# Performance work log

Measured on AMD Instinct MI355X. Metric: run time of the kernel, lower is better.

## Reference

```python
import jax, jax.numpy as jnp
import numpy as np
import math

B, T, D, H = 4, 2048, 1024, 16
DH = D // H

def setup_inputs() -> dict:
    key = jax.random.key(0)
    ks = jax.random.split(key, 12)
    s = 1.0 / math.sqrt(D)
    inp = {
        'q': jax.random.normal(ks[0], (B, T, D), jnp.float32),
        'k': jax.random.normal(ks[1], (B, T, D), jnp.float32),
        'v': jax.random.normal(ks[2], (B, T, D), jnp.float32),
        # causal attn_mask [B, Tq, Tk]; all-keep padding mask [B,1,1,Tk]
        'attn_mask': jnp.broadcast_to(jnp.tril(jnp.ones((T, T), jnp.bool_)), (B, T, T)),
        'key_keep_mask': jnp.ones((B, 1, 1, T), jnp.bool_),
        'wq_w': jax.random.normal(ks[3], (D, D), jnp.float32) * s,
        'wq_b': jnp.zeros((D,), jnp.float32),
        'wk_w': jax.random.normal(ks[4], (D, D), jnp.float32) * s,
        'wk_b': jnp.zeros((D,), jnp.float32),
        'wv_w': jax.random.normal(ks[5], (D, D), jnp.float32) * s,
        'wv_b': jnp.zeros((D,), jnp.float32),
        'wo_w': jax.random.normal(ks[6], (D, D), jnp.float32) * s,
        'wo_b': jnp.zeros((D,), jnp.float32),
    }
    return inp

def reference(q, k, v, attn_mask, key_keep_mask, wq_w, wq_b, wk_w, wk_b, wv_w, wv_b, wo_w, wo_b):
    # projections (torch Linear: x @ W^T + b)
    Q = (q @ wq_w.T + wq_b).reshape(B, -1, H, DH).transpose(0, 2, 1, 3)  # [B,H,Tq,DH]
    K = (k @ wk_w.T + wk_b).reshape(B, -1, H, DH).transpose(0, 2, 1, 3)
    V = (v @ wv_w.T + wv_b).reshape(B, -1, H, DH).transpose(0, 2, 1, 3)
    scores = jnp.einsum('bhqd,bhkd->bhqk', Q, K) / math.sqrt(DH)
    neg_inf = jnp.array(-jnp.inf, scores.dtype)
    scores = jnp.where(attn_mask[:, None, :, :], scores, neg_inf)
    scores = jnp.where(key_keep_mask, scores, neg_inf)
    attn = jax.nn.softmax(scores, axis=-1)  # dropout p=0 -> identity
    out = jnp.einsum('bhqk,bhkd->bhqd', attn, V)
    out = out.transpose(0, 2, 1, 3).reshape(B, -1, D)
    return out @ wo_w.T + wo_b
```

## Files before the change

### kernel.cpp

```cpp
#include <hip/hip_runtime.h>
#include <cstdint>
#include <cstddef>


typedef float f32x4 __attribute__((ext_vector_type(4)));
typedef short bf16x8 __attribute__((ext_vector_type(8)));
typedef float fltx4 __attribute__((ext_vector_type(4)));
typedef unsigned short u16x4 __attribute__((ext_vector_type(4)));

#define GLOBAL_AS __attribute__((address_space(1)))
#define LDS_AS __attribute__((address_space(3)))

__device__ __forceinline__ unsigned short f2bf(float f) {
    union { float f; unsigned int u; } x;
    x.f = f;
    unsigned int u = x.u;
    unsigned int r = (u + 0x7FFFu + ((u >> 16) & 1u)) >> 16;
    return (unsigned short)r;
}

__device__ __forceinline__ unsigned int pack_trunc(float a, float b) {
    union { float f; unsigned int u; } x, y;
    x.f = a; y.f = b;
    return (x.u >> 16) | (y.u & 0xFFFF0000u);
}

__global__ __launch_bounds__(256) void cast_all_kernel(
    const float* __restrict__ q, const float* __restrict__ k, const float* __restrict__ v,
    const float* __restrict__ wq, const float* __restrict__ wk,
    const float* __restrict__ wv, const float* __restrict__ wo,
    unsigned short* __restrict__ dst)
{
    const size_t SEG = 8388608;
    const size_t WSEG = 1048576;
    size_t i = ((size_t)blockIdx.x * 256 + threadIdx.x) * 4;
    const float* src;
    size_t off;
    if (i < SEG)               { src = q;  off = i; }
    else if (i < 2 * SEG)      { src = k;  off = i - SEG; }
    else if (i < 3 * SEG)      { src = v;  off = i - 2 * SEG; }
    else if (i < 3 * SEG + WSEG)     { src = wq; off = i - 3 * SEG; }
    else if (i < 3 * SEG + 2 * WSEG) { src = wk; off = i - 3 * SEG - WSEG; }
    else if (i < 3 * SEG + 3 * WSEG) { src = wv; off = i - 3 * SEG - 2 * WSEG; }
    else                             { src = wo; off = i - 3 * SEG - 3 * WSEG; }
    fltx4 val = *(const fltx4*)(src + off);
    u16x4 o;
    o[0] = f2bf(val[0]);
    o[1] = f2bf(val[1]);
    o[2] = f2bf(val[2]);
    o[3] = f2bf(val[3]);
    *(u16x4*)(dst + i) = o;
}

__global__ __launch_bounds__(256) void qkv_gemm_kernel(
    const unsigned short* __restrict__ X,
    const unsigned short* __restrict__ Wc,
    const float* __restrict__ bq, const float* __restrict__ bk,
    const float* __restrict__ bv,
    unsigned short* __restrict__ Outs,
    float qscale)
{
    const int z = blockIdx.z;
    const unsigned short* A  = X  + (size_t)z * 8388608;
    const unsigned short* Bw = Wc + (size_t)z * 1048576;
    const float* bias = (z == 0) ? bq : (z == 1) ? bk : bv;
    unsigned short* outp = Outs + (size_t)z * 8388608;
    const float scale = (z == 0) ? qscale : 1.0f;
    const bool vmode = (z == 2);

    __shared__ __align__(16) unsigned short lA[128 * 32];
    __shared__ __align__(16) unsigned short lB[128 * 32];
    const int tid = threadIdx.x;
    const int w = tid >> 6, lane = tid & 63;
    const int quad = lane >> 4, l16 = lane & 15;

    const int lin = blockIdx.x + (blockIdx.y << 3);
    const int r_ = lin & 7, s_ = lin >> 3;
    const int bm = ((r_ << 3) | (s_ & 7)) * 128;
    const int bn = (s_ >> 3) * 128;

    const int wm = (w >> 1) * 64, wn = (w & 1) * 64;

    f32x4 acc[4][4] = {};
    const int srow0 = w * 16 + (lane >> 2);

    for (int kb = 0; kb < 32; ++kb) {
        const unsigned short* Ab = A + (size_t)bm * 1024 + kb * 32;
        const unsigned short* Bb = Bw + (size_t)bn * 1024 + kb * 32;
#pragma unroll
        for (int i = 0; i < 2; ++i) {
            int row = i * 64 + srow0;
            int gcb = (lane & 3) ^ ((row >> 1) & 3);
            __builtin_amdgcn_global_load_lds(
                (const GLOBAL_AS unsigned int*)(Ab + (size_t)row * 1024 + gcb * 8),
                (LDS_AS unsigned int*)(lA + i * 2048 + w * 512), 16, 0, 0);
            __builtin_amdgcn_global_load_lds(
                (const GLOBAL_AS unsigned int*)(Bb + (size_t)row * 1024 + gcb * 8),
                (LDS_AS unsigned int*)(lB + i * 2048 + w * 512), 16, 0, 0);
        }
        __syncthreads();

        bf16x8 af[4], bfr[4];
#pragma unroll
        for (int mi = 0; mi < 4; ++mi) {
            int row = wm + mi * 16 + l16;
            af[mi] = *(const bf16x8*)(lA + row * 32 + ((quad ^ ((row >> 1) & 3)) * 8));
        }
#pragma unroll
        for (int ni = 0; ni < 4; ++ni) {
            int row = wn + ni * 16 + l16;
            bfr[ni] = *(const bf16x8*)(lB + row * 32 + ((quad ^ ((row >> 1) & 3)) * 8));
        }
#pragma unroll
        for (int mi = 0; mi < 4; ++mi)
#pragma unroll
            for (int ni = 0; ni < 4; ++ni)
                acc[mi][ni] = __builtin_amdgcn_mfma_f32_16x16x32_bf16(af[mi], bfr[ni], acc[mi][ni], 0, 0, 0);
        __syncthreads();
    }

#pragma unroll
    for (int mi = 0; mi < 4; ++mi) {
        int rowb = bm + wm + mi * 16 + quad * 4;
#pragma unroll
        for (int ni = 0; ni < 4; ++ni) {
            int col = bn + wn + ni * 16 + l16;
            float bv_ = bias[col];
#pragma unroll
            for (int r = 0; r < 4; ++r) {
                int m = rowb + r;
                float vout = (acc[mi][ni][r] + bv_) * scale;
                int b = m >> 11, t = m & 2047, h = col >> 6, d = col & 63;
                if (!vmode) {
                    outp[((size_t)(b * 16 + h) * 2048 + t) * 64 + d] = f2bf(vout);
                } else {
                    outp[((size_t)(b * 16 + h) * 64 + d) * 2048 + t] = f2bf(vout);
                }
            }
        }
    }
}

__global__ __launch_bounds__(256) void out_gemm_kernel(
    const unsigned short* __restrict__ A,
    const unsigned short* __restrict__ Bw,
    const float* __restrict__ bias,
    float* __restrict__ outp)
{
    __shared__ __align__(16) unsigned short lA[128 * 32];
    __shared__ __align__(16) unsigned short lB[128 * 32];
    const int tid = threadIdx.x;
    const int w = tid >> 6, lane = tid & 63;
    const int quad = lane >> 4, l16 = lane & 15;

    const int lin = blockIdx.x + (blockIdx.y << 3);
    const int r_ = lin & 7, s_ = lin >> 3;
    const int bm = ((r_ << 3) | (s_ & 7)) * 128;
    const int bn = (s_ >> 3) * 128;

    const int wm = (w >> 1) * 64, wn = (w & 1) * 64;

    f32x4 acc[4][4] = {};
    const int srow0 = w * 16 + (lane >> 2);

    for (int kb = 0; kb < 32; ++kb) {
        const unsigned short* Ab = A + (size_t)bm * 1024 + kb * 32;
        const unsigned short* Bb = Bw + (size_t)bn * 1024 + kb * 32;
#pragma unroll
        for (int i = 0; i < 2; ++i) {
            int row = i * 64 + srow0;
            int gcb = (lane & 3) ^ ((row >> 1) & 3);
            __builtin_amdgcn_global_load_lds(
                (const GLOBAL_AS unsigned int*)(Ab + (size_t)row * 1024 + gcb * 8),
                (LDS_AS unsigned int*)(lA + i * 2048 + w * 512), 16, 0, 0);
            __builtin_amdgcn_global_load_lds(
                (const GLOBAL_AS unsigned int*)(Bb + (size_t)row * 1024 + gcb * 8),
                (LDS_AS unsigned int*)(lB + i * 2048 + w * 512), 16, 0, 0);
        }
        __syncthreads();

        bf16x8 af[4], bfr[4];
#pragma unroll
        for (int mi = 0; mi < 4; ++mi) {
            int row = wm + mi * 16 + l16;
            af[mi] = *(const bf16x8*)(lA + row * 32 + ((quad ^ ((row >> 1) & 3)) * 8));
        }
#pragma unroll
        for (int ni = 0; ni < 4; ++ni) {
            int row = wn + ni * 16 + l16;
            bfr[ni] = *(const bf16x8*)(lB + row * 32 + ((quad ^ ((row >> 1) & 3)) * 8));
        }
#pragma unroll
        for (int mi = 0; mi < 4; ++mi)
#pragma unroll
            for (int ni = 0; ni < 4; ++ni)
                acc[mi][ni] = __builtin_amdgcn_mfma_f32_16x16x32_bf16(af[mi], bfr[ni], acc[mi][ni], 0, 0, 0);
        __syncthreads();
    }

#pragma unroll
    for (int mi = 0; mi < 4; ++mi) {
        int rowb = bm + wm + mi * 16 + quad * 4;
#pragma unroll
        for (int ni = 0; ni < 4; ++ni) {
            int col = bn + wn + ni * 16 + l16;
            float bv_ = bias[col];
#pragma unroll
            for (int r = 0; r < 4; ++r)
                outp[(size_t)(rowb + r) * 1024 + col] = acc[mi][ni][r] + bv_;
        }
    }
}

__global__ __launch_bounds__(256) void attn_kernel(
    const unsigned short* __restrict__ Qh,
    const unsigned short* __restrict__ Kh,
    const unsigned short* __restrict__ Vt,
    unsigned short* __restrict__ att)
{
    const int tid = threadIdx.x;
    const int w = tid >> 6, lane = tid & 63;
    const int qd = lane >> 4, l16 = lane & 15;
    const int bh = blockIdx.x;
    const int pairy = blockIdx.y;

    const unsigned short* Qp = Qh + (size_t)bh * 2048 * 64;
    const unsigned short* Kp = Kh + (size_t)bh * 2048 * 64;
    const unsigned short* Vp = Vt + (size_t)bh * 64 * 2048;
    const int b = bh >> 4, h = bh & 15;

    __shared__ __align__(16) unsigned short Kl[2][64 * 64];
    __shared__ __align__(16) unsigned short Vl[2][64 * 64];
    __shared__ __align__(16) unsigned short Pl[4][2][16 * 64];

    auto stage = [&](int kt, int buf) {
#pragma unroll
        for (int j = 0; j < 2; ++j) {
            int r = w * 16 + j * 8 + (lane >> 3);
            int c = (lane & 7) ^ (r & 7);
            __builtin_amdgcn_global_load_lds(
                (const GLOBAL_AS unsigned int*)(Kp + (size_t)(kt * 64 + r) * 64 + c * 8),
                (LDS_AS unsigned int*)(&Kl[buf][(w * 16 + j * 8) * 64]), 16, 0, 0);
            __builtin_amdgcn_global_load_lds(
                (const GLOBAL_AS unsigned int*)(Vp + (size_t)r * 2048 + kt * 64 + c * 8),
                (LDS_AS unsigned int*)(&Vl[buf][(w * 16 + j * 8) * 64]), 16, 0, 0);
        }
    };

    auto run_phase = [&](int qblk) {
        const int wqbase = qblk * 128 + w * 32;
        const int ktmax = 2 * qblk + 1;

        bf16x8 qa[2][2];
#pragma unroll
        for (int qt = 0; qt < 2; ++qt)
#pragma unroll
            for (int ks = 0; ks < 2; ++ks)
                qa[qt][ks] = *(const bf16x8*)(Qp + (size_t)(wqbase + qt * 16 + l16) * 64 + ks * 32 + qd * 8);

        float lp[2] = {0.0f, 0.0f};
        f32x4 O[2][4] = {};

        __syncthreads();
        stage(0, 0);

        for (int kt = 0; kt <= ktmax; ++kt) {
            __syncthreads();
            if (kt < ktmax) stage(kt + 1, (kt + 1) & 1);

            if (kt * 64 <= wqbase + 31) {
                const unsigned short* kl = &Kl[kt & 1][0];
                const unsigned short* vl = &Vl[kt & 1][0];

                bf16x8 kf[4][2];
#pragma unroll
                for (int nt = 0; nt < 4; ++nt)
#pragma unroll
                    for (int ks = 0; ks < 2; ++ks)
                        kf[nt][ks] = *(const bf16x8*)(kl + (nt * 16 + l16) * 64 +
                                                      (((ks * 4 + qd) ^ (l16 & 7)) * 8));

                f32x4 S[2][4];
#pragma unroll
                for (int qt = 0; qt < 2; ++qt)
#pragma unroll
                    for (int nt = 0; nt < 4; ++nt) {
                        f32x4 a = {};
                        a = __builtin_amdgcn_mfma_f32_16x16x32_bf16(kf[nt][0], qa[qt][0], a, 0, 0, 0);
                        a = __builtin_amdgcn_mfma_f32_16x16x32_bf16(kf[nt][1], qa[qt][1], a, 0, 0, 0);
                        S[qt][nt] = a;
                    }

                if (kt * 64 + 63 > wqbase) {
#pragma unroll
                    for (int qt = 0; qt < 2; ++qt) {
                        int qrow = wqbase + qt * 16 + l16;
#pragma unroll
                        for (int nt = 0; nt < 4; ++nt) {
                            int kbase = kt * 64 + nt * 16 + qd * 4;
#pragma unroll
                            for (int r = 0; r < 4; ++r)
                                if (kbase + r > qrow) S[qt][nt][r] = -INFINITY;
                        }
                    }
                }

#pragma unroll
                for (int qt = 0; qt < 2; ++qt) {
                    float s0 = 0.0f;
#pragma unroll
                    for (int nt = 0; nt < 4; ++nt)
#pragma unroll
                        for (int r = 0; r < 4; ++r) {
                            float e = __builtin_amdgcn_exp2f(S[qt][nt][r]);
                            S[qt][nt][r] = e;
                            s0 += e;
                        }
                    lp[qt] += s0;
                }

#pragma unroll
                for (int qt = 0; qt < 2; ++qt) {
                    unsigned short* pw = &Pl[w][qt][0];
#pragma unroll
                    for (int nt = 0; nt < 4; ++nt) {
                        uint2 pv;
                        pv.x = pack_trunc(S[qt][nt][0], S[qt][nt][1]);
                        pv.y = pack_trunc(S[qt][nt][2], S[qt][nt][3]);
                        int chunk = (2 * nt + (qd >> 1)) ^ (l16 & 7);
                        *(uint2*)(pw + l16 * 64 + chunk * 8 + (qd & 1) * 4) = pv;
                    }
                }
                asm volatile("s_waitcnt lgkmcnt(0)" ::: "memory");

                bf16x8 pa[2][2];
#pragma unroll
                for (int qt = 0; qt < 2; ++qt)
#pragma unroll
                    for (int s = 0; s < 2; ++s)
                        pa[qt][s] = *(const bf16x8*)(&Pl[w][qt][0] + l16 * 64 +
                                                     (((s * 4 + qd) ^ (l16 & 7)) * 8));

                bf16x8 vf[2][4];
#pragma unroll
                for (int s = 0; s < 2; ++s)
#pragma unroll
                    for (int dh = 0; dh < 4; ++dh)
                        vf[s][dh] = *(const bf16x8*)(vl + (dh * 16 + l16) * 64 +
                                                     (((s * 4 + qd) ^ (l16 & 7)) * 8));
#pragma unroll
                for (int qt = 0; qt < 2; ++qt)
#pragma unroll
                    for (int dh = 0; dh < 4; ++dh) {
                        O[qt][dh] = __builtin_amdgcn_mfma_f32_16x16x32_bf16(pa[qt][0], vf[0][dh], O[qt][dh], 0, 0, 0);
                        O[qt][dh] = __builtin_amdgcn_mfma_f32_16x16x32_bf16(pa[qt][1], vf[1][dh], O[qt][dh], 0, 0, 0);
                    }
            }
        }

#pragma unroll
        for (int qt = 0; qt < 2; ++qt) {
            float lsum = lp[qt];
            lsum += __shfl_xor(lsum, 16, 64);
            lsum += __shfl_xor(lsum, 32, 64);
            float linv = 1.0f / lsum;
#pragma unroll
            for (int r = 0; r < 4; ++r) {
                float lC = __shfl(linv, qd * 4 + r, 64);
                int t = wqbase + qt * 16 + qd * 4 + r;
#pragma unroll
                for (int dh = 0; dh < 4; ++dh) {
                    size_t idx = (size_t)(b * 2048 + t) * 1024 + h * 64 + dh * 16 + l16;
                    att[idx] = f2bf(O[qt][dh][r] * lC);
                }
            }
        }
    };

    run_phase(15 - pairy);
    run_phase(pairy);
}

extern "C" void kernel_launch(void* const* d_in, const int* in_sizes, int n_in,
                              void* d_out, int out_size, void* d_ws, size_t ws_size,
                              hipStream_t stream)
{
    const float* q = (const float*)d_in[0];
    const float* k = (const float*)d_in[1];
    const float* v = (const float*)d_in[2];
    const float* wq_w = (const float*)d_in[5];
    const float* wq_b = (const float*)d_in[6];
    const float* wk_w = (const float*)d_in[7];
    const float* wk_b = (const float*)d_in[8];
    const float* wv_w = (const float*)d_in[9];
    const float* wv_b = (const float*)d_in[10];
    const float* wo_w = (const float*)d_in[11];
    const float* wo_b = (const float*)d_in[12];

    unsigned short* ws = (unsigned short*)d_ws;
    unsigned short* xq  = ws;
    unsigned short* wqc = ws + 25165824;
    unsigned short* woc = ws + 28311552;
    unsigned short* Qhp = ws + 29360128;
    unsigned short* Khp = ws + 37748736;
    unsigned short* Vtp = ws + 46137344;
    unsigned short* att = xq;

    (void)in_sizes; (void)n_in; (void)out_size; (void)ws_size;

    cast_all_kernel<<<28672, 256, 0, stream>>>(q, k, v, wq_w, wk_w, wv_w, wo_w, ws);

    qkv_gemm_kernel<<<dim3(8, 64, 3), 256, 0, stream>>>(
        xq, wqc, wq_b, wk_b, wv_b, Qhp, 0.1803368801f);

    attn_kernel<<<dim3(64, 8), 256, 0, stream>>>(Qhp, Khp, Vtp, att);

    out_gemm_kernel<<<dim3(8, 64), 256, 0, stream>>>(att, woc, wo_b, (float*)d_out);
}
```

Before: 353.2 us.

## Triple-buffer GEMM K-loop with async LDS loads and larger 256x128 tiles

Both projection GEMMs move from a single-buffered 128x128 tile with BK=32 to a 256x128 tile with BK=64, run by 512 threads. Global-to-LDS loads are triple-buffered and issued two stages ahead, with explicit vmcnt waits so memory traffic overlaps the MFMA work. The change also adds an XOR swizzle for the 64-wide rows and raises wave priority around the MFMA block. The cost is 144KB of LDS per block, which limits occupancy, and the correctness of the hand-counted waitcnt values.

```diff
diff --git a/kernel.cpp b/kernel.cpp
--- a/kernel.cpp
+++ b/kernel.cpp
@@ -52,7 +52,8 @@
     *(u16x4*)(dst + i) = o;
 }
 
-__global__ __launch_bounds__(256) void qkv_gemm_kernel(
+
+__global__ __launch_bounds__(512, 2) void qkv_gemm_kernel(
     const unsigned short* __restrict__ X,
     const unsigned short* __restrict__ Wc,
     const float* __restrict__ bq, const float* __restrict__ bk,
@@ -60,7 +61,7 @@
     unsigned short* __restrict__ Outs,
     float qscale)
 {
-    const int z = blockIdx.z;
+    const int z = blockIdx.y;
     const unsigned short* A  = X  + (size_t)z * 8388608;
     const unsigned short* Bw = Wc + (size_t)z * 1048576;
     const float* bias = (z == 0) ? bq : (z == 1) ? bk : bv;
@@ -68,63 +69,96 @@
     const float scale = (z == 0) ? qscale : 1.0f;
     const bool vmode = (z == 2);
 
-    __shared__ __align__(16) unsigned short lA[128 * 32];
-    __shared__ __align__(16) unsigned short lB[128 * 32];
+    __shared__ __align__(16) unsigned short lds[3 * 24576];
+
     const int tid = threadIdx.x;
     const int w = tid >> 6, lane = tid & 63;
     const int quad = lane >> 4, l16 = lane & 15;
-
-    const int lin = blockIdx.x + (blockIdx.y << 3);
+    const int wr = w >> 1, wc = w & 1;
+
+    const int lin = blockIdx.x;
     const int r_ = lin & 7, s_ = lin >> 3;
-    const int bm = ((r_ << 3) | (s_ & 7)) * 128;
-    const int bn = (s_ >> 3) * 128;
-
-    const int wm = (w >> 1) * 64, wn = (w & 1) * 64;
+    const int bm = (r_ * 4 + (s_ & 3)) * 256;
+    const int bn = (s_ >> 2) * 128;
+
+    const int rsub = lane >> 3;
+    const int csw = (lane & 7) ^ rsub;
+
+    auto stage = [&](int kt, int buf) {
+        unsigned short* lA = lds + buf * 24576;
+        unsigned short* lB = lA + 16384;
+        const unsigned short* Ab = A + (size_t)bm * 1024 + kt * 64;
+        const unsigned short* Bb = Bw + (size_t)bn * 1024 + kt * 64;
+#pragma unroll
+        for (int j = 0; j < 4; ++j) {
+            int r0 = w * 32 + j * 8;
+            __builtin_amdgcn_global_load_lds(
+                (const GLOBAL_AS unsigned int*)(Ab + (size_t)(r0 + rsub) * 1024 + csw * 8),
+                (LDS_AS unsigned int*)(lA + r0 * 64), 16, 0, 0);
+        }
+#pragma unroll
+        for (int j = 0; j < 2; ++j) {
+            int r0 = w * 16 + j * 8;
+            __builtin_amdgcn_global_load_lds(
+                (const GLOBAL_AS unsigned int*)(Bb + (size_t)(r0 + rsub) * 1024 + csw * 8),
+                (LDS_AS unsigned int*)(lB + r0 * 64), 16, 0, 0);
+        }
+    };
 
     f32x4 acc[4][4] = {};
-    const int srow0 = w * 16 + (lane >> 2);
-
-    for (int kb = 0; kb < 32; ++kb) {
-        const unsigned short* Ab = A + (size_t)bm * 1024 + kb * 32;
-        const unsigned short* Bb = Bw + (size_t)bn * 1024 + kb * 32;
-#pragma unroll
-        for (int i = 0; i < 2; ++i) {
-            int row = i * 64 + srow0;
-            int gcb = (lane & 3) ^ ((row >> 1) & 3);
-            __builtin_amdgcn_global_load_lds(
-                (const GLOBAL_AS unsigned int*)(Ab + (size_t)row * 1024 + gcb * 8),
-                (LDS_AS unsigned int*)(lA + i * 2048 + w * 512), 16, 0, 0);
-            __builtin_amdgcn_global_load_lds(
-                (const GLOBAL_AS unsigned int*)(Bb + (size_t)row * 1024 + gcb * 8),
-                (LDS_AS unsigned int*)(lB + i * 2048 + w * 512), 16, 0, 0);
-        }
-        __syncthreads();
-
-        bf16x8 af[4], bfr[4];
-#pragma unroll
-        for (int mi = 0; mi < 4; ++mi) {
-            int row = wm + mi * 16 + l16;
-            af[mi] = *(const bf16x8*)(lA + row * 32 + ((quad ^ ((row >> 1) & 3)) * 8));
-        }
+
+    stage(0, 0);
+    stage(1, 1);
+
+    for (int kt = 0; kt < 16; ++kt) {
+        const int cur = kt % 3;
+        if (kt < 14) {
+            stage(kt + 2, (kt + 2) % 3);
+            asm volatile("s_waitcnt vmcnt(12)" ::: "memory");
+        } else if (kt == 14) {
+            asm volatile("s_waitcnt vmcnt(6)" ::: "memory");
+        } else {
+            asm volatile("s_waitcnt vmcnt(0)" ::: "memory");
+        }
+        __builtin_amdgcn_s_barrier();
+        __builtin_amdgcn_sched_barrier(0);
+
+        const unsigned short* lA = lds + cur * 24576;
+        const unsigned short* lB = lA + 16384;
+#pragma unroll
+        for (int kh = 0; kh < 2; ++kh) {
+            bf16x8 af[4], bfr[4];
+#pragma unroll
+            for (int mi = 0; mi < 4; ++mi) {
+                int row = wr * 64 + mi * 16 + l16;
+                af[mi] = *(const bf16x8*)(lA + (size_t)row * 64 +
+                                          (((kh * 4 + quad) ^ (row & 7)) * 8));
+            }
+#pragma unroll
+            for (int ni = 0; ni < 4; ++ni) {
+                int row = wc * 64 + ni * 16 + l16;
+                bfr[ni] = *(const bf16x8*)(lB + (size_t)row * 64 +
+                                           (((kh * 4 + quad) ^ (row & 7)) * 8));
+            }
+            __builtin_amdgcn_s_setprio(1);
+#pragma unroll
+            for (int mi = 0; mi < 4; ++mi)
+#pragma unroll
+                for (int ni = 0; ni < 4; ++ni)
+                    acc[mi][ni] = __builtin_amdgcn_mfma_f32_16x16x32_bf16(
+                        af[mi], bfr[ni], acc[mi][ni], 0, 0, 0);
+            __builtin_amdgcn_s_setprio(0);
+        }
+        __builtin_amdgcn_sched_barrier(0);
+        __builtin_amdgcn_s_barrier();
+    }
+
+#pragma unroll
+    for (int mi = 0; mi < 4; ++mi) {
+        int rowb = bm + wr * 64 + mi * 16 + quad * 4;
 #pragma unroll
         for (int ni = 0; ni < 4; ++ni) {
-            int row = wn + ni * 16 + l16;
-            bfr[ni] = *(const bf16x8*)(lB + row * 32 + ((quad ^ ((row >> 1) & 3)) * 8));
-        }
-#pragma unroll
-        for (int mi = 0; mi < 4; ++mi)
-#pragma unroll
-            for (int ni = 0; ni < 4; ++ni)
-                acc[mi][ni] = __builtin_amdgcn_mfma_f32_16x16x32_bf16(af[mi], bfr[ni], acc[mi][ni], 0, 0, 0);
-        __syncthreads();
-    }
-
-#pragma unroll
-    for (int mi = 0; mi < 4; ++mi) {
-        int rowb = bm + wm + mi * 16 + quad * 4;
-#pragma unroll
-        for (int ni = 0; ni < 4; ++ni) {
-            int col = bn + wn + ni * 16 + l16;
+            int col = bn + wc * 64 + ni * 16 + l16;
             float bv_ = bias[col];
 #pragma unroll
             for (int r = 0; r < 4; ++r) {
@@ -141,69 +175,102 @@
     }
 }
 
-__global__ __launch_bounds__(256) void out_gemm_kernel(
+__global__ __launch_bounds__(512, 2) void out_gemm_kernel(
     const unsigned short* __restrict__ A,
     const unsigned short* __restrict__ Bw,
     const float* __restrict__ bias,
     float* __restrict__ outp)
 {
-    __shared__ __align__(16) unsigned short lA[128 * 32];
-    __shared__ __align__(16) unsigned short lB[128 * 32];
+    __shared__ __align__(16) unsigned short lds[3 * 24576];
+
     const int tid = threadIdx.x;
     const int w = tid >> 6, lane = tid & 63;
     const int quad = lane >> 4, l16 = lane & 15;
-
-    const int lin = blockIdx.x + (blockIdx.y << 3);
+    const int wr = w >> 1, wc = w & 1;
+
+    const int lin = blockIdx.x;
     const int r_ = lin & 7, s_ = lin >> 3;
-    const int bm = ((r_ << 3) | (s_ & 7)) * 128;
-    const int bn = (s_ >> 3) * 128;
-
-    const int wm = (w >> 1) * 64, wn = (w & 1) * 64;
+    const int bm = (r_ * 4 + (s_ & 3)) * 256;
+    const int bn = (s_ >> 2) * 128;
+
+    const int rsub = lane >> 3;
+    const int csw = (lane & 7) ^ rsub;
+
+    auto stage = [&](int kt, int buf) {
+        unsigned short* lA = lds + buf * 24576;
+        unsigned short* lB = lA + 16384;
+        const unsigned short* Ab = A + (size_t)bm * 1024 + kt * 64;
+        const unsigned short* Bb = Bw + (size_t)bn * 1024 + kt * 64;
+#pragma unroll
+        for (int j = 0; j < 4; ++j) {
+            int r0 = w * 32 + j * 8;
+            __builtin_amdgcn_global_load_lds(
+                (const GLOBAL_AS unsigned int*)(Ab + (size_t)(r0 + rsub) * 1024 + csw * 8),
+                (LDS_AS unsigned int*)(lA + r0 * 64), 16, 0, 0);
+        }
+#pragma unroll
+        for (int j = 0; j < 2; ++j) {
+            int r0 = w * 16 + j * 8;
+            __builtin_amdgcn_global_load_lds(
+                (const GLOBAL_AS unsigned int*)(Bb + (size_t)(r0 + rsub) * 1024 + csw * 8),
+                (LDS_AS unsigned int*)(lB + r0 * 64), 16, 0, 0);
+        }
+    };
 
     f32x4 acc[4][4] = {};
-    const int srow0 = w * 16 + (lane >> 2);
-
-    for (int kb = 0; kb < 32; ++kb) {
-        const unsigned short* Ab = A + (size_t)bm * 1024 + kb * 32;
-        const unsigned short* Bb = Bw + (size_t)bn * 1024 + kb * 32;
-#pragma unroll
-        for (int i = 0; i < 2; ++i) {
-            int row = i * 64 + srow0;
-            int gcb = (lane & 3) ^ ((row >> 1) & 3);
-            __builtin_amdgcn_global_load_lds(
-                (const GLOBAL_AS unsigned int*)(Ab + (size_t)row * 1024 + gcb * 8),
-                (LDS_AS unsigned int*)(lA + i * 2048 + w * 512), 16, 0, 0);
-            __builtin_amdgcn_global_load_lds(
-                (const GLOBAL_AS unsigned int*)(Bb + (size_t)row * 1024 + gcb * 8),
-                (LDS_AS unsigned int*)(lB + i * 2048 + w * 512), 16, 0, 0);
-        }
-        __syncthreads();
-
-        bf16x8 af[4], bfr[4];
-#pragma unroll
-        for (int mi = 0; mi < 4; ++mi) {
-            int row = wm + mi * 16 + l16;
-            af[mi] = *(const bf16x8*)(lA + row * 32 + ((quad ^ ((row >> 1) & 3)) * 8));
-        }
+
+    stage(0, 0);
+    stage(1, 1);
+
+    for (int kt = 0; kt < 16; ++kt) {
+        const int cur = kt % 3;
+        if (kt < 14) {
+            stage(kt + 2, (kt + 2) % 3);
+            asm volatile("s_waitcnt vmcnt(12)" ::: "memory");
+        } else if (kt == 14) {
+            asm volatile("s_waitcnt vmcnt(6)" ::: "memory");
+        } else {
+            asm volatile("s_waitcnt vmcnt(0)" ::: "memory");
+        }
+        __builtin_amdgcn_s_barrier();
+        __builtin_amdgcn_sched_barrier(0);
+
+        const unsigned short* lA = lds + cur * 24576;
+        const unsigned short* lB = lA + 16384;
+#pragma unroll
+        for (int kh = 0; kh < 2; ++kh) {
+            bf16x8 af[4], bfr[4];
+#pragma unroll
+            for (int mi = 0; mi < 4; ++mi) {
+                int row = wr * 64 + mi * 16 + l16;
+                af[mi] = *(const bf16x8*)(lA + (size_t)row * 64 +
+                                          (((kh * 4 + quad) ^ (row & 7)) * 8));
+            }
+#pragma unroll
+            for (int ni = 0; ni < 4; ++ni) {
+                int row = wc * 64 + ni * 16 + l16;
+                bfr[ni] = *(const bf16x8*)(lB + (size_t)row * 64 +
+                                           (((kh * 4 + quad) ^ (row & 7)) * 8));
+            }
+            __builtin_amdgcn_s_setprio(1);
+#pragma unroll
+            for (int mi = 0; mi < 4; ++mi)
+#pragma unroll
+                for (int ni = 0; ni < 4; ++ni)
+                    acc[mi][ni] = __builtin_amdgcn_mfma_f32_16x16x32_bf16(
+                        af[mi], bfr[ni], acc[mi][ni], 0, 0, 0);
+            __builtin_amdgcn_s_setprio(0);
+        }
+        __builtin_amdgcn_sched_barrier(0);
+        __builtin_amdgcn_s_barrier();
+    }
+
+#pragma unroll
+    for (int mi = 0; mi < 4; ++mi) {
+        int rowb = bm + wr * 64 + mi * 16 + quad * 4;
 #pragma unroll
         for (int ni = 0; ni < 4; ++ni) {
-            int row = wn + ni * 16 + l16;
-            bfr[ni] = *(const bf16x8*)(lB + row * 32 + ((quad ^ ((row >> 1) & 3)) * 8));
-        }
-#pragma unroll
-        for (int mi = 0; mi < 4; ++mi)
-#pragma unroll
-            for (int ni = 0; ni < 4; ++ni)
-                acc[mi][ni] = __builtin_amdgcn_mfma_f32_16x16x32_bf16(af[mi], bfr[ni], acc[mi][ni], 0, 0, 0);
-        __syncthreads();
-    }
-
-#pragma unroll
-    for (int mi = 0; mi < 4; ++mi) {
-        int rowb = bm + wm + mi * 16 + quad * 4;
-#pragma unroll
-        for (int ni = 0; ni < 4; ++ni) {
-            int col = bn + wn + ni * 16 + l16;
+            int col = bn + wc * 64 + ni * 16 + l16;
             float bv_ = bias[col];
 #pragma unroll
             for (int r = 0; r < 4; ++r)
@@ -410,10 +477,10 @@
 
     cast_all_kernel<<<28672, 256, 0, stream>>>(q, k, v, wq_w, wk_w, wv_w, wo_w, ws);
 
-    qkv_gemm_kernel<<<dim3(8, 64, 3), 256, 0, stream>>>(
+    qkv_gemm_kernel<<<dim3(256, 3), 512, 0, stream>>>(
         xq, wqc, wq_b, wk_b, wv_b, Qhp, 0.1803368801f);
 
     attn_kernel<<<dim3(64, 8), 256, 0, stream>>>(Qhp, Khp, Vtp, att);
 
-    out_gemm_kernel<<<dim3(8, 64), 256, 0, stream>>>(att, woc, wo_b, (float*)d_out);
-}
+    out_gemm_kernel<<<dim3(256), 512, 0, stream>>>(att, woc, wo_b, (float*)d_out);
+}
```

Measured after the change: 349.7 us. No clear change (-1.0%).
